# Optimization experiments

Hardware: AMD Instinct MI355X
Metric: run time of the kernel (lower is better)

The kernel has to match this reference:

```python
import jax, jax.numpy as jnp
import numpy as np

N_NODES = 100000
N_EDGES = 1600000
IN_C, HID_C, OUT_C = 19, 128, 4


def setup_inputs() -> dict:
    key = jax.random.key(0)
    ks = jax.random.split(key, 8)
    x = jax.random.normal(ks[0], (N_NODES, IN_C), dtype=jnp.float32)
    edge_index = jax.random.randint(ks[1], (2, N_EDGES), 0, N_NODES, dtype=jnp.int64)
    def glorot(k, shape):
        lim = np.sqrt(6.0 / (shape[0] + shape[1]))
        return jax.random.uniform(k, shape, jnp.float32, -lim, lim)
    return {
        "x": x,
        "edge_index": edge_index,
        "w1_l": glorot(ks[2], (IN_C, HID_C)),
        "w1_r": glorot(ks[3], (IN_C, HID_C)),
        "b1": jnp.zeros((HID_C,), jnp.float32),
        "w2_l": glorot(ks[4], (HID_C, OUT_C)),
        "w2_r": glorot(ks[5], (HID_C, OUT_C)),
        "b2": jnp.zeros((OUT_C,), jnp.float32),
    }


def _sage_conv(x, edge_index, w_l, w_r, b):
    # PyG SAGEConv (mean aggr): out = mean_{j in N(i)} x_j @ w_l + x_i @ w_r + b
    src, dst = edge_index[0], edge_index[1]
    n = x.shape[0]
    msg = x[src]                                            # [E, C] gather
    agg = jax.ops.segment_sum(msg, dst, num_segments=n)     # [N, C] scatter-add
    cnt = jax.ops.segment_sum(jnp.ones((src.shape[0],), x.dtype), dst, num_segments=n)
    mean = agg / jnp.maximum(cnt, 1.0)[:, None]
    return mean @ w_l + x @ w_r + b


def reference(x, edge_index, w1_l, w1_r, b1, w2_l, w2_r, b2):
    h = _sage_conv(x, edge_index, w1_l, w1_r, b1)
    h = jax.nn.relu(h)
    # dropout omitted (eval/inference mode reference)
    out = _sage_conv(h, edge_index, w2_l, w2_r, b2)
    return jax.nn.log_softmax(out, axis=1)
```

## Files before the change

### kernel.cpp

```cpp
#include <hip/hip_runtime.h>
#include <math.h>


constexpr int N    = 100000;
constexpr int E    = 1600000;
constexpr int INC  = 19;
constexpr int HID  = 128;
constexpr int OUTC = 4;
constexpr int WS   = 52;

constexpr int BSH    = 8;
constexpr int BMASK  = 255;
constexpr int NBUK   = (N + 255) >> BSH;
constexpr int BCAP   = 6144;
constexpr int BA_BLK = 256;
constexpr int CHUNK  = (E + BA_BLK - 1) / BA_BLK;
constexpr int CPT    = (CHUNK + 255) / 256;

__device__ inline float bf2f(unsigned short u) {
    return __uint_as_float((unsigned)u << 16);
}

__device__ inline unsigned short f2bf(float f) {
    unsigned u = __float_as_uint(f);
    u += 0x7FFFu + ((u >> 16) & 1u);
    return (unsigned short)(u >> 16);
}

__global__ void detect_pack(const int* __restrict__ ei, int* __restrict__ flag,
                            int* __restrict__ gcnt,
                            const float* __restrict__ x, float* __restrict__ xp,
                            unsigned short* __restrict__ xph,
                            const float* __restrict__ w1l, const float* __restrict__ w1r,
                            const float* __restrict__ b1,  const float* __restrict__ w2l,
                            const float* __restrict__ w2r, float* __restrict__ WT) {
    int tid = blockIdx.x * blockDim.x + threadIdx.x;
    if (tid < N * 20) {
        int node = tid / 20;
        int c    = tid - node * 20;
        float v = (c < INC) ? x[(size_t)node * INC + c] : 0.f;
        xp[tid] = v;
        xph[tid] = f2bf(v);
    }
    if (blockIdx.x == 0) {
        __shared__ int any;
        if (threadIdx.x == 0) any = 0;
        __syncthreads();
        for (int k = threadIdx.x; k < 512; k += 256) gcnt[k] = 0;
        int v = 0;
        for (int k = threadIdx.x; k < 1024; k += 256)
            v |= ei[2 * k + 1];
        if (v) atomicOr(&any, 1);
        __syncthreads();
        if (threadIdx.x == 0) *flag = (any == 0) ? 1 : 0;
    } else if (blockIdx.x == 1) {
        int o = threadIdx.x;
        if (o < HID) {
            float* w = WT + o * WS;
            for (int c = 0; c < INC; ++c) {
                w[c]      = w1l[c * HID + o];
                w[20 + c] = w1r[c * HID + o];
            }
            w[19] = 0.f;
            w[39] = 0.f;
            for (int k = 0; k < OUTC; ++k) {
                w[40 + k] = w2l[o * OUTC + k];
                w[44 + k] = w2r[o * OUTC + k];
            }
            w[48] = b1[o];
            w[49] = 0.f; w[50] = 0.f; w[51] = 0.f;
        }
    }
}

__global__ __launch_bounds__(256) void bin_kernel(const int* __restrict__ ei,
                                                  const int* __restrict__ flag,
                                                  int* __restrict__ gcnt,
                                                  unsigned* __restrict__ be) {
    __shared__ int cnt[NBUK];
    __shared__ int base[NBUK];
    int t = threadIdx.x;
    for (int k = t; k < NBUK; k += 256) cnt[k] = 0;
    __syncthreads();

    int is64 = *flag;
    int lo = blockIdx.x * CHUNK;
    int hi = lo + CHUNK; if (hi > E) hi = E;

    int dstv[CPT];
#pragma unroll
    for (int k = 0; k < CPT; ++k) {
        int e = lo + k * 256 + t;
        int dv = 0;
        if (e < hi) {
            dv = is64 ? ei[2 * E + 2 * e] : ei[E + e];
            atomicAdd(&cnt[dv >> BSH], 1);
        }
        dstv[k] = dv;
    }
    __syncthreads();

    for (int k = t; k < NBUK; k += 256) {
        base[k] = atomicAdd(&gcnt[k], cnt[k]);
        cnt[k] = 0;
    }
    __syncthreads();

#pragma unroll
    for (int k = 0; k < CPT; ++k) {
        int e = lo + k * 256 + t;
        if (e < hi) {
            int dst = dstv[k];
            int src = is64 ? ei[2 * e] : ei[e];
            int b = dst >> BSH;
            int r = atomicAdd(&cnt[b], 1);
            int pos = base[b] + r;
            if (pos < BCAP)
                be[(size_t)b * BCAP + pos] =
                    ((unsigned)(dst & BMASK) << 17) | (unsigned)src;
        }
    }
}

__global__ __launch_bounds__(256) void bucket_csr(const unsigned* __restrict__ be,
                                                  const int* __restrict__ gcnt,
                                                  int* __restrict__ adj,
                                                  int* __restrict__ deg,
                                                  int* __restrict__ start) {
    __shared__ int hist[256];
    __shared__ int sloc[256];
    __shared__ int cur[256];
    __shared__ int gbs;
    int b = blockIdx.x;
    int t = threadIdx.x;

    hist[t] = 0;
    cur[t]  = 0;
    if (t == 0) gbs = 0;
    __syncthreads();

    int part = 0;
    for (int i = t; i < b; i += 256) part += gcnt[i];
    if (part) atomicAdd(&gbs, part);

    int sz = gcnt[b]; if (sz > BCAP) sz = BCAP;
    const unsigned* bp = be + (size_t)b * BCAP;

    for (int i = t; i < sz; i += 256) {
        int dl = bp[i] >> 17;
        atomicAdd(&hist[dl], 1);
    }
    __syncthreads();

    int v = hist[t];
    sloc[t] = v;
    __syncthreads();
    for (int off = 1; off < 256; off <<= 1) {
        int add = (t >= off) ? sloc[t - off] : 0;
        __syncthreads();
        sloc[t] += add;
        __syncthreads();
    }
    int sl = sloc[t] - v;

    int gb = gbs;
    int node = b * 256 + t;
    if (node < N) {
        deg[node]   = v;
        start[node] = gb + sl;
    }
    __syncthreads();

    for (int i = t; i < sz; i += 256) {
        unsigned p = bp[i];
        int dl  = p >> 17;
        int src = (int)(p & 0x1FFFFu);
        int r = atomicAdd(&cur[dl], 1);
        adj[gb + (sloc[dl] - hist[dl]) + r] = src;
    }
}

__global__ void gather_bf16(const ushort4* __restrict__ xph4,
                            const int* __restrict__ adj,
                            const int* __restrict__ start,
                            const int* __restrict__ deg,
                            float4* __restrict__ mean1p4) {
    int tid = blockIdx.x * blockDim.x + threadIdx.x;
    if (tid >= N * 5) return;
    int node = tid / 5;
    int q    = tid - node * 5;
    int d  = deg[node];
    int st = start[node];
    float4 a0 = make_float4(0.f, 0.f, 0.f, 0.f);
    float4 a1 = a0, a2 = a0, a3 = a0;
    int j = 0;
    for (; j + 7 < d; j += 8) {
        int s0 = adj[st + j];
        int s1 = adj[st + j + 1];
        int s2 = adj[st + j + 2];
        int s3 = adj[st + j + 3];
        int s4 = adj[st + j + 4];
        int s5 = adj[st + j + 5];
        int s6 = adj[st + j + 6];
        int s7 = adj[st + j + 7];
        ushort4 u0 = xph4[(size_t)s0 * 5 + q];
        ushort4 u1 = xph4[(size_t)s1 * 5 + q];
        ushort4 u2 = xph4[(size_t)s2 * 5 + q];
        ushort4 u3 = xph4[(size_t)s3 * 5 + q];
        ushort4 u4 = xph4[(size_t)s4 * 5 + q];
        ushort4 u5 = xph4[(size_t)s5 * 5 + q];
        ushort4 u6 = xph4[(size_t)s6 * 5 + q];
        ushort4 u7 = xph4[(size_t)s7 * 5 + q];
        a0.x += bf2f(u0.x); a0.y += bf2f(u0.y); a0.z += bf2f(u0.z); a0.w += bf2f(u0.w);
        a1.x += bf2f(u1.x); a1.y += bf2f(u1.y); a1.z += bf2f(u1.z); a1.w += bf2f(u1.w);
        a2.x += bf2f(u2.x); a2.y += bf2f(u2.y); a2.z += bf2f(u2.z); a2.w += bf2f(u2.w);
        a3.x += bf2f(u3.x); a3.y += bf2f(u3.y); a3.z += bf2f(u3.z); a3.w += bf2f(u3.w);
        a0.x += bf2f(u4.x); a0.y += bf2f(u4.y); a0.z += bf2f(u4.z); a0.w += bf2f(u4.w);
        a1.x += bf2f(u5.x); a1.y += bf2f(u5.y); a1.z += bf2f(u5.z); a1.w += bf2f(u5.w);
        a2.x += bf2f(u6.x); a2.y += bf2f(u6.y); a2.z += bf2f(u6.z); a2.w += bf2f(u6.w);
        a3.x += bf2f(u7.x); a3.y += bf2f(u7.y); a3.z += bf2f(u7.z); a3.w += bf2f(u7.w);
    }
    for (; j + 3 < d; j += 4) {
        int s0 = adj[st + j];
        int s1 = adj[st + j + 1];
        int s2 = adj[st + j + 2];
        int s3 = adj[st + j + 3];
        ushort4 u0 = xph4[(size_t)s0 * 5 + q];
        ushort4 u1 = xph4[(size_t)s1 * 5 + q];
        ushort4 u2 = xph4[(size_t)s2 * 5 + q];
        ushort4 u3 = xph4[(size_t)s3 * 5 + q];
        a0.x += bf2f(u0.x); a0.y += bf2f(u0.y); a0.z += bf2f(u0.z); a0.w += bf2f(u0.w);
        a1.x += bf2f(u1.x); a1.y += bf2f(u1.y); a1.z += bf2f(u1.z); a1.w += bf2f(u1.w);
        a2.x += bf2f(u2.x); a2.y += bf2f(u2.y); a2.z += bf2f(u2.z); a2.w += bf2f(u2.w);
        a3.x += bf2f(u3.x); a3.y += bf2f(u3.y); a3.z += bf2f(u3.z); a3.w += bf2f(u3.w);
    }
    for (; j < d; ++j) {
        ushort4 u = xph4[(size_t)adj[st + j] * 5 + q];
        a0.x += bf2f(u.x); a0.y += bf2f(u.y); a0.z += bf2f(u.z); a0.w += bf2f(u.w);
    }
    float inv = 1.0f / fmaxf((float)d, 1.0f);
    float4 m;
    m.x = ((a0.x + a1.x) + (a2.x + a3.x)) * inv;
    m.y = ((a0.y + a1.y) + (a2.y + a3.y)) * inv;
    m.z = ((a0.z + a1.z) + (a2.z + a3.z)) * inv;
    m.w = ((a0.w + a1.w) + (a2.w + a3.w)) * inv;
    mean1p4[(size_t)node * 5 + q] = m;
}

__global__ __launch_bounds__(256) void dense_v6(
        const float4* __restrict__ xp4,
        const float4* __restrict__ mean1p4,
        const float* __restrict__ WT,
        float* __restrict__ g,
        float* __restrict__ s) {
    __shared__ float P[3][64 * 9];

    int t    = threadIdx.x;
    int lane = t & 63;
    int part = __builtin_amdgcn_readfirstlane(t >> 6);
    int node = blockIdx.x * 64 + lane;
    bool valid = node < N;

    float msp[20], xsp[20];
#pragma unroll
    for (int q = 0; q < 5; ++q) {
        float4 mv = valid ? mean1p4[(size_t)node * 5 + q] : make_float4(0.f, 0.f, 0.f, 0.f);
        float4 xv = valid ? xp4[(size_t)node * 5 + q]     : make_float4(0.f, 0.f, 0.f, 0.f);
        msp[4 * q] = mv.x; msp[4 * q + 1] = mv.y; msp[4 * q + 2] = mv.z; msp[4 * q + 3] = mv.w;
        xsp[4 * q] = xv.x; xsp[4 * q + 1] = xv.y; xsp[4 * q + 2] = xv.z; xsp[4 * q + 3] = xv.w;
    }

    float r[8] = {0.f, 0.f, 0.f, 0.f, 0.f, 0.f, 0.f, 0.f};
    int o0 = part * 32;
#pragma unroll 2
    for (int oo = 0; oo < 32; ++oo) {
        int o = o0 + oo;
        const float* __restrict__ w = WT + o * WS;
        float a0 = 0.f, a1 = 0.f, a2 = 0.f, a3 = 0.f;
#pragma unroll
        for (int q = 0; q < 5; ++q) {
            a0 += msp[4 * q]     * w[4 * q]      + xsp[4 * q]     * w[20 + 4 * q];
            a1 += msp[4 * q + 1] * w[4 * q + 1]  + xsp[4 * q + 1] * w[21 + 4 * q];
            a2 += msp[4 * q + 2] * w[4 * q + 2]  + xsp[4 * q + 2] * w[22 + 4 * q];
            a3 += msp[4 * q + 3] * w[4 * q + 3]  + xsp[4 * q + 3] * w[23 + 4 * q];
        }
        float h = fmaxf(((a0 + a1) + (a2 + a3)) + w[48], 0.0f);
        r[0] += h * w[40]; r[1] += h * w[41]; r[2] += h * w[42]; r[3] += h * w[43];
        r[4] += h * w[44]; r[5] += h * w[45]; r[6] += h * w[46]; r[7] += h * w[47];
    }

    if (part != 0) {
        float* p = &P[part - 1][lane * 9];
#pragma unroll
        for (int k = 0; k < 8; ++k) p[k] = r[k];
    }
    __syncthreads();

    if (part == 0 && valid) {
#pragma unroll
        for (int k = 0; k < 8; ++k)
            r[k] = ((r[k] + P[0][lane * 9 + k]) + P[1][lane * 9 + k])
                   + P[2][lane * 9 + k];
        *(float4*)(g + (size_t)node * OUTC) = make_float4(r[0], r[1], r[2], r[3]);
        *(float4*)(s + (size_t)node * OUTC) = make_float4(r[4], r[5], r[6], r[7]);
    }
}

__global__ void final_v3(const float* __restrict__ g,
                         const int* __restrict__ adj,
                         const int* __restrict__ start,
                         const int* __restrict__ deg,
                         const float* __restrict__ s,
                         const float* __restrict__ b2,
                         float* __restrict__ out) {
    int tid  = blockIdx.x * blockDim.x + threadIdx.x;
    int node = tid >> 2;
    int l    = tid & 3;
    if (node >= N) return;
    int d  = deg[node];
    int st = start[node];
    float ax = 0.f, ay = 0.f, az = 0.f, aw = 0.f;
    for (int j = l; j < d; j += 4) {
        int sn = adj[st + j];
        const float4 gv = *(const float4*)(g + (size_t)sn * OUTC);
        ax += gv.x; ay += gv.y; az += gv.z; aw += gv.w;
    }
    ax += __shfl_down(ax, 2, 4); ay += __shfl_down(ay, 2, 4);
    az += __shfl_down(az, 2, 4); aw += __shfl_down(aw, 2, 4);
    ax += __shfl_down(ax, 1, 4); ay += __shfl_down(ay, 1, 4);
    az += __shfl_down(az, 1, 4); aw += __shfl_down(aw, 1, 4);
    if (l == 0) {
        float inv = 1.0f / fmaxf((float)d, 1.0f);
        const float4 sv = *(const float4*)(s + (size_t)node * OUTC);
        float o0 = ax * inv + sv.x + b2[0];
        float o1 = ay * inv + sv.y + b2[1];
        float o2 = az * inv + sv.z + b2[2];
        float o3 = aw * inv + sv.w + b2[3];
        float m = fmaxf(fmaxf(o0, o1), fmaxf(o2, o3));
        float sum = expf(o0 - m) + expf(o1 - m) + expf(o2 - m) + expf(o3 - m);
        float lse = logf(sum) + m;
        *(float4*)(out + (size_t)node * OUTC) =
            make_float4(o0 - lse, o1 - lse, o2 - lse, o3 - lse);
    }
}

extern "C" void kernel_launch(void* const* d_in, const int* in_sizes, int n_in,
                              void* d_out, int out_size, void* d_ws, size_t ws_size,
                              hipStream_t stream) {
    const float* x   = (const float*)d_in[0];
    const int*   ei  = (const int*)d_in[1];
    const float* w1l = (const float*)d_in[2];
    const float* w1r = (const float*)d_in[3];
    const float* b1  = (const float*)d_in[4];
    const float* w2l = (const float*)d_in[5];
    const float* w2r = (const float*)d_in[6];
    const float* b2  = (const float*)d_in[7];
    float* out = (float*)d_out;

    int*            ws    = (int*)d_ws;
    int*            flag  = ws;
    int*            gcnt  = ws + 64;
    int*            deg   = gcnt + 512;
    int*            start = deg + N;
    unsigned*       be    = (unsigned*)(start + N);
    int*            adj   = (int*)(be + (size_t)NBUK * BCAP);
    float*          g     = (float*)(adj + E);
    float*          s     = g + (size_t)N * OUTC;
    float*          xp    = s + (size_t)N * OUTC;
    unsigned short* xph   = (unsigned short*)(xp + (size_t)N * 20);
    float*          mean1p= (float*)(xph + (size_t)N * 20);
    float*          WT    = mean1p + (size_t)N * 20;

    detect_pack<<<(N * 20 + 255) / 256, 256, 0, stream>>>(
        ei, flag, gcnt, x, xp, xph, w1l, w1r, b1, w2l, w2r, WT);
    bin_kernel<<<BA_BLK, 256, 0, stream>>>(ei, flag, gcnt, be);
    bucket_csr<<<NBUK, 256, 0, stream>>>(be, gcnt, adj, deg, start);
    gather_bf16<<<(N * 5 + 255) / 256, 256, 0, stream>>>(
        (const ushort4*)xph, adj, start, deg, (float4*)mean1p);
    dense_v6<<<(N + 63) / 64, 256, 0, stream>>>(
        (const float4*)xp, (const float4*)mean1p, WT, g, s);
    final_v3<<<(N * 4 + 255) / 256, 256, 0, stream>>>(g, adj, start, deg, s, b2, out);
}
```

Baseline: 112.3 us.

## Fuse input packing and int64 detection into binning kernel; widen final aggregation

```diff
diff --git a/kernel.cpp b/kernel.cpp
--- a/kernel.cpp
+++ b/kernel.cpp
@@ -27,65 +27,62 @@
     return (unsigned short)(u >> 16);
 }
 
-__global__ void detect_pack(const int* __restrict__ ei, int* __restrict__ flag,
-                            int* __restrict__ gcnt,
-                            const float* __restrict__ x, float* __restrict__ xp,
-                            unsigned short* __restrict__ xph,
-                            const float* __restrict__ w1l, const float* __restrict__ w1r,
-                            const float* __restrict__ b1,  const float* __restrict__ w2l,
-                            const float* __restrict__ w2r, float* __restrict__ WT) {
-    int tid = blockIdx.x * blockDim.x + threadIdx.x;
-    if (tid < N * 20) {
-        int node = tid / 20;
-        int c    = tid - node * 20;
-        float v = (c < INC) ? x[(size_t)node * INC + c] : 0.f;
-        xp[tid] = v;
-        xph[tid] = f2bf(v);
-    }
-    if (blockIdx.x == 0) {
-        __shared__ int any;
-        if (threadIdx.x == 0) any = 0;
-        __syncthreads();
-        for (int k = threadIdx.x; k < 512; k += 256) gcnt[k] = 0;
-        int v = 0;
-        for (int k = threadIdx.x; k < 1024; k += 256)
-            v |= ei[2 * k + 1];
-        if (v) atomicOr(&any, 1);
-        __syncthreads();
-        if (threadIdx.x == 0) *flag = (any == 0) ? 1 : 0;
-    } else if (blockIdx.x == 1) {
-        int o = threadIdx.x;
-        if (o < HID) {
-            float* w = WT + o * WS;
-            for (int c = 0; c < INC; ++c) {
-                w[c]      = w1l[c * HID + o];
-                w[20 + c] = w1r[c * HID + o];
-            }
-            w[19] = 0.f;
-            w[39] = 0.f;
-            for (int k = 0; k < OUTC; ++k) {
-                w[40 + k] = w2l[o * OUTC + k];
-                w[44 + k] = w2r[o * OUTC + k];
-            }
-            w[48] = b1[o];
-            w[49] = 0.f; w[50] = 0.f; w[51] = 0.f;
-        }
-    }
-}
-
 __global__ __launch_bounds__(256) void bin_kernel(const int* __restrict__ ei,
-                                                  const int* __restrict__ flag,
                                                   int* __restrict__ gcnt,
-                                                  unsigned* __restrict__ be) {
+                                                  unsigned* __restrict__ be,
+                                                  const float* __restrict__ x,
+                                                  float* __restrict__ xp,
+                                                  unsigned short* __restrict__ xph,
+                                                  const float* __restrict__ w1l,
+                                                  const float* __restrict__ w1r,
+                                                  const float* __restrict__ b1,
+                                                  const float* __restrict__ w2l,
+                                                  const float* __restrict__ w2r,
+                                                  float* __restrict__ WT) {
     __shared__ int cnt[NBUK];
     __shared__ int base[NBUK];
+    __shared__ int anyv;
     int t = threadIdx.x;
+
+    for (int k = blockIdx.x * 256 + t; k < N * 20; k += BA_BLK * 256) {
+        int node = k / 20;
+        int c    = k - node * 20;
+        float v = (c < INC) ? x[(size_t)node * INC + c] : 0.f;
+        xp[k] = v;
+        xph[k] = f2bf(v);
+    }
+    if (blockIdx.x == 0 && t < HID) {
+        int o = t;
+        float* w = WT + o * WS;
+        for (int c = 0; c < INC; ++c) {
+            w[c]      = w1l[c * HID + o];
+            w[20 + c] = w1r[c * HID + o];
+        }
+        w[19] = 0.f;
+        w[39] = 0.f;
+        for (int k = 0; k < OUTC; ++k) {
+            w[40 + k] = w2l[o * OUTC + k];
+            w[44 + k] = w2r[o * OUTC + k];
+        }
+        w[48] = b1[o];
+        w[49] = 0.f; w[50] = 0.f; w[51] = 0.f;
+    }
+
+    if (t == 0) anyv = 0;
     for (int k = t; k < NBUK; k += 256) cnt[k] = 0;
     __syncthreads();
 
-    int is64 = *flag;
     int lo = blockIdx.x * CHUNK;
     int hi = lo + CHUNK; if (hi > E) hi = E;
+
+    {
+        int v = 0;
+        for (int e = lo + t; e < hi; e += 256)
+            v |= ei[2 * e + 1];
+        if (v) atomicOr(&anyv, 1);
+    }
+    __syncthreads();
+    int is64 = (anyv == 0) ? 1 : 0;
 
     int dstv[CPT];
 #pragma unroll
@@ -306,7 +303,7 @@
     }
 }
 
-__global__ void final_v3(const float* __restrict__ g,
+__global__ void final_v4(const float* __restrict__ g,
                          const int* __restrict__ adj,
                          const int* __restrict__ start,
                          const int* __restrict__ deg,
@@ -314,21 +311,23 @@
                          const float* __restrict__ b2,
                          float* __restrict__ out) {
     int tid  = blockIdx.x * blockDim.x + threadIdx.x;
-    int node = tid >> 2;
-    int l    = tid & 3;
+    int node = tid >> 3;
+    int l    = tid & 7;
     if (node >= N) return;
     int d  = deg[node];
     int st = start[node];
     float ax = 0.f, ay = 0.f, az = 0.f, aw = 0.f;
-    for (int j = l; j < d; j += 4) {
+    for (int j = l; j < d; j += 8) {
         int sn = adj[st + j];
         const float4 gv = *(const float4*)(g + (size_t)sn * OUTC);
         ax += gv.x; ay += gv.y; az += gv.z; aw += gv.w;
     }
-    ax += __shfl_down(ax, 2, 4); ay += __shfl_down(ay, 2, 4);
-    az += __shfl_down(az, 2, 4); aw += __shfl_down(aw, 2, 4);
-    ax += __shfl_down(ax, 1, 4); ay += __shfl_down(ay, 1, 4);
-    az += __shfl_down(az, 1, 4); aw += __shfl_down(aw, 1, 4);
+    ax += __shfl_down(ax, 4, 8); ay += __shfl_down(ay, 4, 8);
+    az += __shfl_down(az, 4, 8); aw += __shfl_down(aw, 4, 8);
+    ax += __shfl_down(ax, 2, 8); ay += __shfl_down(ay, 2, 8);
+    az += __shfl_down(az, 2, 8); aw += __shfl_down(aw, 2, 8);
+    ax += __shfl_down(ax, 1, 8); ay += __shfl_down(ay, 1, 8);
+    az += __shfl_down(az, 1, 8); aw += __shfl_down(aw, 1, 8);
     if (l == 0) {
         float inv = 1.0f / fmaxf((float)d, 1.0f);
         const float4 sv = *(const float4*)(s + (size_t)node * OUTC);
@@ -358,8 +357,7 @@
     float* out = (float*)d_out;
 
     int*            ws    = (int*)d_ws;
-    int*            flag  = ws;
-    int*            gcnt  = ws + 64;
+    int*            gcnt  = ws;
     int*            deg   = gcnt + 512;
     int*            start = deg + N;
     unsigned*       be    = (unsigned*)(start + N);
@@ -371,13 +369,13 @@
     float*          mean1p= (float*)(xph + (size_t)N * 20);
     float*          WT    = mean1p + (size_t)N * 20;
 
-    detect_pack<<<(N * 20 + 255) / 256, 256, 0, stream>>>(
-        ei, flag, gcnt, x, xp, xph, w1l, w1r, b1, w2l, w2r, WT);
-    bin_kernel<<<BA_BLK, 256, 0, stream>>>(ei, flag, gcnt, be);
+    hipMemsetAsync(gcnt, 0, 512 * sizeof(int), stream);
+    bin_kernel<<<BA_BLK, 256, 0, stream>>>(ei, gcnt, be, x, xp, xph,
+                                           w1l, w1r, b1, w2l, w2r, WT);
     bucket_csr<<<NBUK, 256, 0, stream>>>(be, gcnt, adj, deg, start);
     gather_bf16<<<(N * 5 + 255) / 256, 256, 0, stream>>>(
         (const ushort4*)xph, adj, start, deg, (float4*)mean1p);
     dense_v6<<<(N + 63) / 64, 256, 0, stream>>>(
         (const float4*)xp, (const float4*)mean1p, WT, g, s);
-    final_v3<<<(N * 4 + 255) / 256, 256, 0, stream>>>(g, adj, start, deg, s, b2, out);
-}
+    final_v4<<<(N * 8 + 255) / 256, 256, 0, stream>>>(g, adj, start, deg, s, b2, out);
+}
```

Result: slower. 126.5 us (+12.7%).
